# Performance work log

Hardware: AMD Instinct MI355X
Metric: run time of the kernel (lower is better)

The kernel has to match this reference:

```python
import jax, jax.numpy as jnp
import numpy as np

V = 16000      # vocab_size
D = 256        # embedding_dim
H = 512        # hidden_size (bi-LSTM concat)
HD = H // 2    # per-direction hidden
LAB = 32       # labelset_size (30 tags + START/STOP)
T = 512        # seq length
B = 128        # batch
START = 30
STOP = 31
NEG = -10000.0


def setup_inputs() -> dict:
    key = jax.random.key(0)
    ks = jax.random.split(key, 16)
    sc = 0.05
    emb = jax.random.normal(ks[0], (V, D), jnp.float32) * 0.1
    W_ih_f = jax.random.normal(ks[1], (4 * HD, D), jnp.float32) * sc
    W_hh_f = jax.random.normal(ks[2], (4 * HD, HD), jnp.float32) * sc
    b_f = jax.random.normal(ks[3], (4 * HD,), jnp.float32) * sc  # b_ih + b_hh combined
    W_ih_b = jax.random.normal(ks[4], (4 * HD, D), jnp.float32) * sc
    W_hh_b = jax.random.normal(ks[5], (4 * HD, HD), jnp.float32) * sc
    b_b = jax.random.normal(ks[6], (4 * HD,), jnp.float32) * sc
    Wo = jax.random.normal(ks[7], (LAB, H), jnp.float32) * sc
    bo = jnp.zeros((LAB,), jnp.float32)
    transitions = jax.random.normal(ks[8], (LAB, LAB), jnp.float32)
    transitions = transitions.at[STOP, :].set(NEG).at[:, START].set(NEG)
    h0 = jax.random.normal(ks[9], (2, B, HD), jnp.float32)  # init_hidden() uses randn
    c0 = jax.random.normal(ks[10], (2, B, HD), jnp.float32)
    sentences = jax.random.randint(ks[11], (T, B), 0, V, dtype=jnp.int32)
    labels = jax.random.randint(ks[12], (T, B), 0, 30, dtype=jnp.int32)
    masks = jnp.ones((T, B), dtype=bool)
    return {"emb": emb, "W_ih_f": W_ih_f, "W_hh_f": W_hh_f, "b_f": b_f,
            "W_ih_b": W_ih_b, "W_hh_b": W_hh_b, "b_b": b_b,
            "Wo": Wo, "bo": bo, "transitions": transitions,
            "h0": h0, "c0": c0,
            "sentences": sentences, "labels": labels, "masks": masks}


def _lstm_dir(xproj, h0, c0, W_hh):
    # xproj: [T, B, 4*HD] precomputed input projection (+bias)
    def step(carry, xg):
        h, c = carry
        g = xg + h @ W_hh.T
        i, f, gg, o = jnp.split(g, 4, axis=-1)  # torch gate order i,f,g,o
        i = jax.nn.sigmoid(i); f = jax.nn.sigmoid(f)
        gg = jnp.tanh(gg); o = jax.nn.sigmoid(o)
        c = f * c + i * gg
        h = o * jnp.tanh(c)
        return (h, c), h
    _, hs = jax.lax.scan(step, (h0, c0), xproj)
    return hs  # [T, B, HD]


def reference(emb, W_ih_f, W_hh_f, b_f, W_ih_b, W_hh_b, b_b, Wo, bo,
              transitions, h0, c0, sentences, labels, masks):
    # ---- encoder (dropout omitted: eval-mode determinism) ----
    x = emb[sentences]                                   # [T, B, D]
    xf = jnp.einsum('tbd,gd->tbg', x, W_ih_f) + b_f
    hf = _lstm_dir(xf, h0[0], c0[0], W_hh_f)             # [T, B, HD]
    xb = jnp.einsum('tbd,gd->tbg', x, W_ih_b) + b_b
    hb = _lstm_dir(xb[::-1], h0[1], c0[1], W_hh_b)[::-1]
    out = jnp.concatenate([hf, hb], axis=-1)             # [T, B, H]
    feats = jnp.einsum('tbh,lh->tbl', out, Wo) + bo      # [T, B, LAB]

    # ---- CRF forward algorithm (log partition) ----
    dp0 = jnp.full((B, LAB), NEG, jnp.float32).at[:, START].set(0.0)
    def fstep(dp, inp):
        sc, m = inp  # sc: [B, LAB], m: [B]
        new = jax.scipy.special.logsumexp(
            dp[:, :, None] + transitions[None, :, :] + sc[:, None, :], axis=1)
        return jnp.where(m[:, None], new, dp), None
    dpZ, _ = jax.lax.scan(fstep, dp0, (feats, masks))
    Z = jax.scipy.special.logsumexp(dpZ, axis=1)         # [B]

    # ---- gold path score ----
    lab_ext = jnp.concatenate(
        [jnp.full((1, B), START, labels.dtype), labels], axis=0)  # [T+1, B]
    bidx = jnp.arange(B)
    def gstep(dp, inp):
        sc, m, lp, ln = inp
        tmp = dp + transitions[lp, ln] + sc[bidx, ln]
        return jnp.where(m, tmp, dp), None
    gold, _ = jax.lax.scan(gstep, jnp.zeros((B,), jnp.float32),
                           (feats, masks, lab_ext[:-1], lab_ext[1:]))

    return (Z - gold).sum() / B
```

## Files before the change

### kernel.cpp

```cpp
#include <hip/hip_runtime.h>
#include <stdint.h>

typedef __attribute__((ext_vector_type(8))) short short8;
typedef __attribute__((ext_vector_type(4))) float floatx4;
typedef __attribute__((ext_vector_type(8))) int intx8;
typedef __attribute__((ext_vector_type(2))) int intx2;
typedef unsigned int u32;
typedef unsigned short u16;
typedef unsigned long long u64;

#define NROW 65536
#define RING 32

#define OFF_TAGS  64
#define OFF_READY 256
#define OFF_WIH   8192
#define OFF_WHH8  1056768
#define OFF_WO    2105344
#define OFF_RING  2138112
#define OFF_OUT   19177472
#define OFF_FE    86286336
#define WS_NEED   94674944

__device__ __forceinline__ u16 f2bf(float f){
  union { float f; u32 u; } v; v.f = f;
  u32 u = v.u;
  return (u16)((u + 0x7FFFu + ((u >> 16) & 1u)) >> 16);
}
__device__ __forceinline__ float bf2f(u16 h){
  union { u32 u; float f; } v; v.u = ((u32)h) << 16; return v.f;
}
__device__ __forceinline__ u32 pack2(float a, float b){
  return (u32)f2bf(a) | ((u32)f2bf(b) << 16);
}
__device__ __forceinline__ u32 pk_fp8x4(float a, float b, float c, float d){
  u32 lo = __builtin_amdgcn_cvt_pk_fp8_f32(a, b, 0, false);
  return (u32)__builtin_amdgcn_cvt_pk_fp8_f32(c, d, lo, true);
}
__device__ __forceinline__ float sigm(float x){
  return __builtin_amdgcn_rcpf(1.f + __expf(-x));
}
__device__ __forceinline__ float tanh_(float x){
  return 1.f - 2.f * __builtin_amdgcn_rcpf(1.f + __expf(2.f * x));
}
__device__ __forceinline__ floatx4 MF(short8 a, short8 b, floatx4 c){
  return __builtin_amdgcn_mfma_f32_16x16x32_bf16(a, b, c, 0, 0, 0);
}
__device__ __forceinline__ floatx4 MFS(intx8 a, intx8 b, floatx4 c){
  return __builtin_amdgcn_mfma_scale_f32_16x16x128_f8f6f4(
      a, b, c, 0, 0, 0, 0x7F7F7F7F, 0, 0x7F7F7F7F);
}
template<int CTRL>
__device__ __forceinline__ u32 dppq(u32 x){
  return (u32)__builtin_amdgcn_update_dpp(0, (int)x, CTRL, 0xF, 0xF, false);
}
__device__ __forceinline__ void ldsload16(const void* g, void* l){
  __builtin_amdgcn_global_load_lds(
      (const __attribute__((address_space(1))) u32*)g,
      (__attribute__((address_space(3))) u32*)l, 16, 0, 17);
}

__global__ void kdiag(float* out, float v){
  if (threadIdx.x == 0 && blockIdx.x == 0) out[0] = v;
}

__global__ void k0(const float* wf, const float* wb, const float* hf, const float* hb,
                   const float* wo, u16* wih, u16* wob, unsigned char* whh8){
  int e = blockIdx.x * 256 + threadIdx.x;
  if (e < 524288){ wih[e] = f2bf(e < 262144 ? wf[e] : wb[e - 262144]); return; }
  if (e < 540672){ wob[e - 524288] = f2bf(wo[e - 524288]); return; }
  if (e < 1064960){
    int t = e - 540672;
    float w = (t < 262144) ? hf[t] : hb[t - 262144];
    whh8[t] = (unsigned char)(__builtin_amdgcn_cvt_pk_fp8_f32(w, w, 0, false) & 0xFF);
  }
}

__global__ void __launch_bounds__(1024) __attribute__((amdgpu_waves_per_eu(4, 4)))
klstm(const float* emb, const int* sent, const u16* wih,
      const float* bf_, const float* bb_,
      const unsigned char* whh8, const float* h0, const float* c0,
      char* ring, u16* outb, u32* ct, u32* ready){
  __shared__ __align__(16) char SH[98304];
  const int tid = threadIdx.x, w = tid >> 6, l = tid & 63, q = l >> 4, l15 = l & 15;
  const int bid = blockIdx.x;

  if (bid >= 32){
    const int p = bid - 32, dir = p & 1;
    const float* bias = dir ? bb_ : bf_;
    const int m = w & 7, ch = w >> 3;
    int pbud = 1 << 20;
    for (int u = p; u < 1024; u += 224){
      const int s = u >> 1;
      const int t = dir ? 511 - s : s;
      if (s >= 31){
        const int li = l, need = s - 30;
        bool done = false;
        while (!done && pbud > 0){
          int v = need;
          if (li < 16)
            v = (int)__hip_atomic_load(&ct[dir * 16 + li], __ATOMIC_RELAXED, __HIP_MEMORY_SCOPE_AGENT);
          done = (__ballot(v >= need) == ~0ull);
          if (!done){ __builtin_amdgcn_s_sleep(32); pbud--; }
        }
      }
      {
        int r = tid >> 3, g0 = tid & 7;
        const float* er = emb + (size_t)sent[t * 128 + r] * 256;
        #pragma unroll
        for (int j = 0; j < 4; j++){
          int g8 = g0 + j * 8;
          float4 a = *(const float4*)(er + g8 * 8);
          float4 b = *(const float4*)(er + g8 * 8 + 4);
          u32 gg[4] = { pack2(a.x, a.y), pack2(a.z, a.w), pack2(b.x, b.y), pack2(b.z, b.w) };
          *(uint4*)&SH[(g8 * 128 + r) * 16] = *(uint4*)gg;
        }
      }
      __syncthreads();
      short8 Afr[8];
      #pragma unroll
      for (int ks = 0; ks < 8; ks++)
        Afr[ks] = *(const short8*)&SH[((ks * 4 + q) * 128 + m * 16 + l15) * 16];
      char* slot = ring + (size_t)(dir * RING + (s & (RING - 1))) * 262144;
      const int bcw = m * 2 + (q >> 1);
      for (int nt = 0; nt < 16; nt++){
        __syncthreads();
        {
          int r = tid & 63, grp = tid >> 6;
          const u16* wsrc = wih + (size_t)(dir * 1024 + nt * 64 + r) * 256;
          #pragma unroll
          for (int i = 0; i < 2; i++){
            int kg = grp * 2 + i;
            uint4 v = *(const uint4*)(wsrc + kg * 8);
            *(uint4*)&SH[65536 + (kg * 64 + r) * 16] = v;
          }
        }
        __syncthreads();
        floatx4 acc[2];
        acc[0] = floatx4{0.f,0.f,0.f,0.f};
        acc[1] = floatx4{0.f,0.f,0.f,0.f};
        #pragma unroll
        for (int ks = 0; ks < 8; ks++){
          #pragma unroll
          for (int jt = 0; jt < 2; jt++){
            short8 b = *(const short8*)&SH[65536 + ((ks * 4 + q) * 64 + ch * 32 + jt * 16 + l15) * 16];
            acc[jt] = MF(Afr[ks], b, acc[jt]);
          }
        }
        #pragma unroll
        for (int jt = 0; jt < 2; jt++){
          int col = nt * 64 + ch * 32 + jt * 16 + l15;
          float bv = bias[col];
          u32 pr[2] = { pack2(acc[jt][0] + bv, acc[jt][1] + bv),
                        pack2(acc[jt][2] + bv, acc[jt][3] + bv) };
          *(uint2*)(slot + bcw * 16384 + col * 16 + (q & 1) * 8) = *(uint2*)pr;
        }
      }
      asm volatile("s_waitcnt vmcnt(0)" ::: "memory");
      __syncthreads();
      if (tid == 0){
        __builtin_amdgcn_fence(__ATOMIC_RELEASE, "agent");
        __hip_atomic_store(&ready[dir * 512 + s], 1u, __ATOMIC_RELAXED, __HIP_MEMORY_SCOPE_AGENT);
      }
    }
    return;
  }

  const int dir = bid >> 4, bc = bid & 15;
  const int nn = w >> 1, hw = w & 1;
  const int H0 = nn * 32 + hw * 16, hid = H0 + l15;
  const int b0loc = (q & 1) * 4 + (q >> 1) * 2;
  const int i4 = l15 & 3, j4 = l15 >> 2;
  int cbud = 1 << 22;
  const u32 s01 = i4==0?0x00000400u : i4==1?0x00000105u : i4==2?0x06020000u : 0x03070000u;
  const u32 s23 = i4==0?0x04000000u : i4==1?0x01050000u : i4==2?0x00000602u : 0x00000307u;
  const u32 sfn = (i4 < 2) ? 0x07060100u : 0x03020504u;

  intx8 Wf[4][2];
  #pragma unroll
  for (int g = 0; g < 4; g++){
    const unsigned char* wr = whh8 + (size_t)(dir * 1024 + g * 256 + hid) * 256;
    #pragma unroll
    for (int i = 0; i < 2; i++)
      Wf[g][i] = *(const intx8*)(wr + i * 128 + q * 32);
  }
  #pragma unroll
  for (int g = 0; g < 4; g++){
    #pragma unroll
    for (int i = 0; i < 2; i++)
      asm volatile("" : "+v"(Wf[g][i]));
  }
  float creg[2];
  #pragma unroll
  for (int e = 0; e < 2; e++)
    creg[e] = c0[((size_t)dir * 128 + bc * 8 + b0loc + e) * 256 + hid];
  {
    int a = tid * 4;
    int kg = a >> 7, rest = a & 127, b = rest >> 3, off4 = a & 4;
    u32 val0 = 0;
    if (b < 8){
      const float* hr = h0 + ((size_t)dir * 128 + bc * 8 + b) * 256 + kg * 8 + off4;
      val0 = pk_fp8x4(hr[0], hr[1], hr[2], hr[3]);
    }
    *(u32*)&SH[49152 + a] = val0;
    *(u32*)&SH[49152 + 4096 + a] = 0;
  }
  #pragma unroll
  for (int pp = 0; pp < 2; pp++){
    while (__hip_atomic_load(&ready[dir * 512 + pp], __ATOMIC_RELAXED, __HIP_MEMORY_SCOPE_AGENT) == 0u
           && --cbud > 0)
      __builtin_amdgcn_s_sleep(8);
    const char* rp = ring + (size_t)(dir * RING + pp) * 262144 + bc * 16384;
    ldsload16(rp + tid * 16, SH + pp * 16384 + tid * 16);
  }
  u32 rdyv = __hip_atomic_load(&ready[dir * 512 + 2], __ATOMIC_RELAXED, __HIP_MEMORY_SCOPE_AGENT);
  asm volatile("s_waitcnt vmcnt(0)" ::: "memory");
  __syncthreads();

  int xcur = 0, xn2 = 2;
  for (int s = 0; s < 512; s++){
    const int t = dir ? 511 - s : s;
    u32 rdyn = 1u;
    if (s + 3 < 512)
      rdyn = __hip_atomic_load(&ready[dir * 512 + s + 3], __ATOMIC_RELAXED, __HIP_MEMORY_SCOPE_AGENT);
    if (s + 2 < 512){
      if (rdyv == 0u){
        while (__hip_atomic_load(&ready[dir * 512 + s + 2], __ATOMIC_RELAXED, __HIP_MEMORY_SCOPE_AGENT) == 0u
               && --cbud > 0)
          __builtin_amdgcn_s_sleep(2);
      }
      const char* rp = ring + (size_t)(dir * RING + ((s + 2) & (RING - 1))) * 262144 + bc * 16384;
      ldsload16(rp + tid * 16, SH + xn2 * 16384 + tid * 16);
    }
    rdyv = rdyn;

    const char* xb0 = SH + xcur * 16384;
    u32 xg[4];
    #pragma unroll
    for (int g = 0; g < 4; g++)
      xg[g] = *(const u32*)(xb0 + ((g * 256 + hid) * 16 + b0loc * 2));

    const char* hb = SH + 49152 + (s & 1) * 4096;
    floatx4 acc[4];
    #pragma unroll
    for (int g = 0; g < 4; g++) acc[g] = floatx4{0.f,0.f,0.f,0.f};
    #pragma unroll
    for (int i = 0; i < 2; i++){
      union { long l[4]; intx8 v; } au;
      #pragma unroll
      for (int j = 0; j < 4; j++)
        au.l[j] = *(const long*)(hb + ((i * 16 + q * 4 + j) * 16 + l15) * 8);
      #pragma unroll
      for (int g = 0; g < 4; g++)
        acc[g] = MFS(au.v, Wf[g][i], acc[g]);
    }

    float v[4][2];
    #pragma unroll
    for (int g = 0; g < 4; g++)
      #pragma unroll
      for (int e = 0; e < 2; e++){
        union { float f; int i; } lo, hi;
        lo.f = acc[g][e]; hi.f = acc[g][2 + e];
        intx2 r = __builtin_amdgcn_permlane32_swap(lo.i, hi.i, false, false);
        union { int i; float f; } o; o.i = r[0];
        v[g][e] = o.f;
      }

    float hv[2];
    #pragma unroll
    for (int e = 0; e < 2; e++){
      float gi = v[0][e] + bf2f((u16)(xg[0] >> (16 * e)));
      float gf = v[1][e] + bf2f((u16)(xg[1] >> (16 * e)));
      float gg = v[2][e] + bf2f((u16)(xg[2] >> (16 * e)));
      float go = v[3][e] + bf2f((u16)(xg[3] >> (16 * e)));
      gi = sigm(gi); gf = sigm(gf); gg = tanh_(gg); go = sigm(go);
      float c = gf * creg[e] + gi * gg;
      creg[e] = c;
      hv[e] = go * tanh_(c);
      outb[((size_t)t * 128 + bc * 8 + b0loc + e) * 512 + dir * 256 + hid] = f2bf(hv[e]);
    }

    {
      u32 pk = (u32)__builtin_amdgcn_cvt_pk_fp8_f32(hv[0], hv[1], 0, false);
      intx2 rq = __builtin_amdgcn_permlane32_swap((int)pk, (int)pk, false, false);
      u32 quad = (u32)rq[0] | ((u32)rq[1] << 16);
      u32 r1 = dppq<0xB1>(quad);
      u32 r2 = dppq<0x4E>(quad);
      u32 r3 = dppq<0x1B>(quad);
      u32 p01 = __builtin_amdgcn_perm(r1, quad, s01);
      u32 p23 = __builtin_amdgcn_perm(r3, r2, s23);
      u32 outw = __builtin_amdgcn_perm(p23, p01, sfn);
      char* hn = SH + 49152 + ((s + 1) & 1) * 4096;
      if (q < 2){
        int bq = q * 4 + i4;
        int hidg = H0 + j4 * 4;
        *(u32*)&hn[(hidg >> 3) * 128 + bq * 8 + (hidg & 4)] = outw;
      }
    }
    if (tid == 0)
      __hip_atomic_store(&ct[dir * 16 + bc], (u32)(s + 1), __ATOMIC_RELAXED, __HIP_MEMORY_SCOPE_AGENT);

    if (s < 509){
      asm volatile("s_waitcnt vmcnt(4) lgkmcnt(0)" ::: "memory");
      __builtin_amdgcn_s_barrier();
    } else if (s < 511){
      asm volatile("s_waitcnt vmcnt(0)" ::: "memory");
      __syncthreads();
    }
    xcur = (xcur == 2) ? 0 : xcur + 1;
    xn2  = (xn2  == 2) ? 0 : xn2  + 1;
  }
}

__launch_bounds__(256, 2)
__global__ void k5(const u16* outb, const u16* wob, const float* bo, float* fe){
  const int tid = threadIdx.x, w = tid >> 6, l15 = tid & 15, q = (tid >> 4) & 3;
  const int rows0 = blockIdx.x * 64;
  short8 WoF[2][16];
  #pragma unroll
  for (int jt = 0; jt < 2; jt++)
    #pragma unroll
    for (int ks = 0; ks < 16; ks++)
      WoF[jt][ks] = *(const short8*)(wob + (size_t)(jt * 16 + l15) * 512 + ks * 32 + q * 8);
  floatx4 a5[2] = { floatx4{0.f,0.f,0.f,0.f}, floatx4{0.f,0.f,0.f,0.f} };
  const u16* ar = outb + (size_t)(rows0 + w * 16 + l15) * 512;
  #pragma unroll
  for (int ks = 0; ks < 16; ks++){
    short8 a = *(const short8*)(ar + ks * 32 + q * 8);
    a5[0] = MF(a, WoF[0][ks], a5[0]);
    a5[1] = MF(a, WoF[1][ks], a5[1]);
  }
  #pragma unroll
  for (int jt = 0; jt < 2; jt++){
    float bv = bo[jt * 16 + l15];
    #pragma unroll
    for (int rg = 0; rg < 4; rg++)
      fe[(size_t)(rows0 + w * 16 + q * 4 + rg) * 32 + jt * 16 + l15] = a5[jt][rg] + bv;
  }
}

__global__ void k6(const float* fe, const int* labels, const float* trans, float* accp){
  __shared__ float TrL[1024];
  __shared__ __align__(16) float dpL[4][32];
  const int tid = threadIdx.x, w = tid >> 6, l = tid & 63, j = l & 31, half = l >> 5;
  const int b = blockIdx.x * 4 + w;
  for (int i = tid; i < 1024; i += 256) TrL[i] = trans[i];
  __syncthreads();
  float Trl[16];
  #pragma unroll
  for (int ii = 0; ii < 16; ii++) Trl[ii] = TrL[(half * 16 + ii) * 32 + j];
  if (half == 0) dpL[w][j] = (j == 30) ? 0.f : -10000.f;

  float gold = 0.f; int lp = 30;
  float sc = fe[(size_t)b * 32 + j];
  int lab = labels[b];
  float ndF = 0.f;
  for (int t = 0; t < 512; t++){
    float scN = 0.f; int labN = 0;
    if (t < 511){
      scN = fe[((size_t)(t + 1) * 128 + b) * 32 + j];
      labN = labels[(t + 1) * 128 + b];
    }
    float dpv[16], tt[16];
    {
      const float4 a = *(const float4*)&dpL[w][half * 16 + 0];
      const float4 b4 = *(const float4*)&dpL[w][half * 16 + 4];
      const float4 c4 = *(const float4*)&dpL[w][half * 16 + 8];
      const float4 d4 = *(const float4*)&dpL[w][half * 16 + 12];
      dpv[0]=a.x; dpv[1]=a.y; dpv[2]=a.z; dpv[3]=a.w;
      dpv[4]=b4.x; dpv[5]=b4.y; dpv[6]=b4.z; dpv[7]=b4.w;
      dpv[8]=c4.x; dpv[9]=c4.y; dpv[10]=c4.z; dpv[11]=c4.w;
      dpv[12]=d4.x; dpv[13]=d4.y; dpv[14]=d4.z; dpv[15]=d4.w;
    }
    float m = -3.0e38f;
    #pragma unroll
    for (int ii = 0; ii < 16; ii++){ tt[ii] = dpv[ii] + Trl[ii]; m = fmaxf(m, tt[ii]); }
    float M = fmaxf(m, __shfl_xor(m, 32));
    float ssum = 0.f;
    #pragma unroll
    for (int ii = 0; ii < 16; ii++) ssum += __expf(tt[ii] - M);
    ssum += __shfl_xor(ssum, 32);
    float nd = sc + M + __logf(ssum);
    float scl = __shfl(sc, lab);
    gold += TrL[lp * 32 + lab] + scl;
    lp = lab;
    if (half == 0) dpL[w][j] = nd;
    ndF = nd;
    sc = scN; lab = labN;
  }
  float M2 = ndF, S2 = 1.f;
  #pragma unroll
  for (int off = 1; off < 64; off <<= 1){
    float Mo = __shfl_xor(M2, off), So = __shfl_xor(S2, off);
    float Mn = fmaxf(M2, Mo);
    S2 = S2 * __expf(M2 - Mn) + So * __expf(Mo - Mn);
    M2 = Mn;
  }
  float Z = M2 + __logf(S2 * 0.5f);
  if (l == 0) atomicAdd(accp, Z - gold);
}

__global__ void k7(const float* accp, float* out){
  if (threadIdx.x == 0 && blockIdx.x == 0) out[0] = accp[0] * (1.f / 128.f);
}

extern "C" void kernel_launch(void* const* d_in, const int* in_sizes, int n_in,
                              void* d_out, int out_size, void* d_ws, size_t ws_size,
                              hipStream_t stream){
  float* outp = (float*)d_out;
  if (ws_size < (size_t)WS_NEED){
    hipLaunchKernelGGL(kdiag, dim3(1), dim3(64), 0, stream, outp, (float)ws_size);
    return;
  }
  const float* emb  = (const float*)d_in[0];
  const float* Wihf = (const float*)d_in[1];
  const float* Whhf = (const float*)d_in[2];
  const float* bf_  = (const float*)d_in[3];
  const float* Wihb = (const float*)d_in[4];
  const float* Whhb = (const float*)d_in[5];
  const float* bb_  = (const float*)d_in[6];
  const float* Wo   = (const float*)d_in[7];
  const float* bo   = (const float*)d_in[8];
  const float* trans= (const float*)d_in[9];
  const float* h0   = (const float*)d_in[10];
  const float* c0   = (const float*)d_in[11];
  const int*   sent = (const int*)d_in[12];
  const int*   labels = (const int*)d_in[13];

  char* ws = (char*)d_ws;
  float* accp = (float*)ws;
  u32* ct    = (u32*)(ws + OFF_TAGS);
  u32* ready = (u32*)(ws + OFF_READY);
  u16* wih   = (u16*)(ws + OFF_WIH);
  unsigned char* whh8 = (unsigned char*)(ws + OFF_WHH8);
  u16* wob   = (u16*)(ws + OFF_WO);
  char* ring = ws + OFF_RING;
  u16* outb  = (u16*)(ws + OFF_OUT);
  float* fe  = (float*)(ws + OFF_FE);

  hipMemsetAsync(d_ws, 0, 8192, stream);
  hipLaunchKernelGGL(k0, dim3(4160), dim3(256), 0, stream,
                     Wihf, Wihb, Whhf, Whhb, Wo, wih, wob, whh8);
  hipLaunchKernelGGL(klstm, dim3(256), dim3(1024), 0, stream,
                     emb, sent, wih, bf_, bb_, whh8, h0, c0, ring, outb, ct, ready);
  hipLaunchKernelGGL(k5, dim3(1024), dim3(256), 0, stream, outb, wob, bo, fe);
  hipLaunchKernelGGL(k6, dim3(32), dim3(256), 0, stream, fe, labels, trans, accp);
  hipLaunchKernelGGL(k7, dim3(1), dim3(64), 0, stream, accp, outp);
}
```

Baseline: 1.370 ms.

## Load LSTM input projections directly into registers instead of staging through LDS

The producer now writes the precomputed input-gate projections in a per-lane layout (hidden unit × batch-pair, with the four gates contiguous), so each recurrent-step lane can fetch its four gate words straight from the global ring with system-scope atomic loads. The old path, which used a global-to-LDS async copy into three rotating LDS buffers followed by LDS reads, is removed, and the prefetch distance drops from two steps to one. The aim is to take the LDS staging and its read latency off the serial recurrence critical path. In exchange, each step issues more small global loads with less lookahead, and the vmcnt wait accounting has been changed to match.

Result: slower. 1.922 ms (+40.3%).

```diff
diff --git a/kernel.cpp b/kernel.cpp
--- a/kernel.cpp
+++ b/kernel.cpp
@@ -54,10 +54,8 @@
 __device__ __forceinline__ u32 dppq(u32 x){
   return (u32)__builtin_amdgcn_update_dpp(0, (int)x, CTRL, 0xF, 0xF, false);
 }
-__device__ __forceinline__ void ldsload16(const void* g, void* l){
-  __builtin_amdgcn_global_load_lds(
-      (const __attribute__((address_space(1))) u32*)g,
-      (__attribute__((address_space(3))) u32*)l, 16, 0, 17);
+__device__ __forceinline__ u32 ldsys(const u32* p){
+  return __hip_atomic_load(p, __ATOMIC_RELAXED, __HIP_MEMORY_SCOPE_SYSTEM);
 }
 
 __global__ void kdiag(float* out, float v){
@@ -151,9 +149,11 @@
         for (int jt = 0; jt < 2; jt++){
           int col = nt * 64 + ch * 32 + jt * 16 + l15;
           float bv = bias[col];
-          u32 pr[2] = { pack2(acc[jt][0] + bv, acc[jt][1] + bv),
-                        pack2(acc[jt][2] + bv, acc[jt][3] + bv) };
-          *(uint2*)(slot + bcw * 16384 + col * 16 + (q & 1) * 8) = *(uint2*)pr;
+          u32 lo = pack2(acc[jt][0] + bv, acc[jt][1] + bv);
+          u32 hi = pack2(acc[jt][2] + bv, acc[jt][3] + bv);
+          char* base = slot + bcw * 16384 + (size_t)(col & 255) * 64 + (col >> 8) * 4;
+          *(u32*)(base + ((q & 1) * 2 + 0) * 16) = lo;
+          *(u32*)(base + ((q & 1) * 2 + 1) * 16) = hi;
         }
       }
       asm volatile("s_waitcnt vmcnt(0)" ::: "memory");
@@ -170,6 +170,7 @@
   const int nn = w >> 1, hw = w & 1;
   const int H0 = nn * 32 + hw * 16, hid = H0 + l15;
   const int b0loc = (q & 1) * 4 + (q >> 1) * 2;
+  const int bpair = b0loc >> 1;
   const int i4 = l15 & 3, j4 = l15 >> 2;
   int cbud = 1 << 22;
   const u32 s01 = i4==0?0x00000400u : i4==1?0x00000105u : i4==2?0x06020000u : 0x03070000u;
@@ -205,40 +206,37 @@
     *(u32*)&SH[49152 + a] = val0;
     *(u32*)&SH[49152 + 4096 + a] = 0;
   }
-  #pragma unroll
-  for (int pp = 0; pp < 2; pp++){
-    while (__hip_atomic_load(&ready[dir * 512 + pp], __ATOMIC_RELAXED, __HIP_MEMORY_SCOPE_AGENT) == 0u
-           && --cbud > 0)
-      __builtin_amdgcn_s_sleep(8);
-    const char* rp = ring + (size_t)(dir * RING + pp) * 262144 + bc * 16384;
-    ldsload16(rp + tid * 16, SH + pp * 16384 + tid * 16);
-  }
-  u32 rdyv = __hip_atomic_load(&ready[dir * 512 + 2], __ATOMIC_RELAXED, __HIP_MEMORY_SCOPE_AGENT);
+  const size_t lane_off = (size_t)bc * 16384 + (size_t)hid * 64 + (size_t)bpair * 16;
+  while (__hip_atomic_load(&ready[dir * 512 + 0], __ATOMIC_RELAXED, __HIP_MEMORY_SCOPE_AGENT) == 0u
+         && --cbud > 0)
+    __builtin_amdgcn_s_sleep(8);
+  u32 xg[4];
+  {
+    const u32* xp = (const u32*)(ring + (size_t)(dir * RING + 0) * 262144 + lane_off);
+    #pragma unroll
+    for (int g = 0; g < 4; g++) xg[g] = ldsys(xp + g);
+  }
+  u32 rdyv = __hip_atomic_load(&ready[dir * 512 + 1], __ATOMIC_RELAXED, __HIP_MEMORY_SCOPE_AGENT);
   asm volatile("s_waitcnt vmcnt(0)" ::: "memory");
   __syncthreads();
 
-  int xcur = 0, xn2 = 2;
   for (int s = 0; s < 512; s++){
     const int t = dir ? 511 - s : s;
     u32 rdyn = 1u;
-    if (s + 3 < 512)
-      rdyn = __hip_atomic_load(&ready[dir * 512 + s + 3], __ATOMIC_RELAXED, __HIP_MEMORY_SCOPE_AGENT);
-    if (s + 2 < 512){
+    if (s + 2 < 512)
+      rdyn = __hip_atomic_load(&ready[dir * 512 + s + 2], __ATOMIC_RELAXED, __HIP_MEMORY_SCOPE_AGENT);
+    u32 xn[4] = {0u, 0u, 0u, 0u};
+    if (s + 1 < 512){
       if (rdyv == 0u){
-        while (__hip_atomic_load(&ready[dir * 512 + s + 2], __ATOMIC_RELAXED, __HIP_MEMORY_SCOPE_AGENT) == 0u
+        while (__hip_atomic_load(&ready[dir * 512 + s + 1], __ATOMIC_RELAXED, __HIP_MEMORY_SCOPE_AGENT) == 0u
                && --cbud > 0)
           __builtin_amdgcn_s_sleep(2);
       }
-      const char* rp = ring + (size_t)(dir * RING + ((s + 2) & (RING - 1))) * 262144 + bc * 16384;
-      ldsload16(rp + tid * 16, SH + xn2 * 16384 + tid * 16);
+      const u32* xp = (const u32*)(ring + (size_t)(dir * RING + ((s + 1) & (RING - 1))) * 262144 + lane_off);
+      #pragma unroll
+      for (int g = 0; g < 4; g++) xn[g] = ldsys(xp + g);
     }
     rdyv = rdyn;
-
-    const char* xb0 = SH + xcur * 16384;
-    u32 xg[4];
-    #pragma unroll
-    for (int g = 0; g < 4; g++)
-      xg[g] = *(const u32*)(xb0 + ((g * 256 + hid) * 16 + b0loc * 2));
 
     const char* hb = SH + 49152 + (s & 1) * 4096;
     floatx4 acc[4];
@@ -301,15 +299,15 @@
     if (tid == 0)
       __hip_atomic_store(&ct[dir * 16 + bc], (u32)(s + 1), __ATOMIC_RELAXED, __HIP_MEMORY_SCOPE_AGENT);
 
-    if (s < 509){
-      asm volatile("s_waitcnt vmcnt(4) lgkmcnt(0)" ::: "memory");
+    if (s < 510){
+      asm volatile("s_waitcnt vmcnt(2) lgkmcnt(0)" ::: "memory");
       __builtin_amdgcn_s_barrier();
     } else if (s < 511){
       asm volatile("s_waitcnt vmcnt(0)" ::: "memory");
       __syncthreads();
     }
-    xcur = (xcur == 2) ? 0 : xcur + 1;
-    xn2  = (xn2  == 2) ? 0 : xn2  + 1;
+    #pragma unroll
+    for (int g = 0; g < 4; g++) xg[g] = xn[g];
   }
 }
 
```

## Split LSTM recurrence across 64 blocks with 4 batch rows each

Applied to the files above, without the earlier changes.

The recurrent LSTM blocks are doubled from 32 to 64, so each block handles 4 batch rows per direction instead of 8. The ring layout for the input projection changes to per-4-row sub-slots of 8 KB, and each lane now computes one hidden/batch element. That removes the permlane32 swaps and the complex perm shuffle used to repack h. The projection producer blocks shrink from 224 to 192 and wait on 32 counters per direction. Each recurrent step now does less serial work per block, at the cost of fewer producer blocks, wasted MFMA lanes on padded rows, and more synchronisation counters.

Result: slower. 2.707 ms (+97.7%).

```diff
diff --git a/kernel.cpp b/kernel.cpp
--- a/kernel.cpp
+++ b/kernel.cpp
@@ -4,16 +4,14 @@
 typedef __attribute__((ext_vector_type(8))) short short8;
 typedef __attribute__((ext_vector_type(4))) float floatx4;
 typedef __attribute__((ext_vector_type(8))) int intx8;
-typedef __attribute__((ext_vector_type(2))) int intx2;
 typedef unsigned int u32;
 typedef unsigned short u16;
 typedef unsigned long long u64;
 
-#define NROW 65536
 #define RING 32
 
 #define OFF_TAGS  64
-#define OFF_READY 256
+#define OFF_READY 512
 #define OFF_WIH   8192
 #define OFF_WHH8  1056768
 #define OFF_WO    2105344
@@ -85,12 +83,12 @@
   const int tid = threadIdx.x, w = tid >> 6, l = tid & 63, q = l >> 4, l15 = l & 15;
   const int bid = blockIdx.x;
 
-  if (bid >= 32){
-    const int p = bid - 32, dir = p & 1;
+  if (bid >= 64){
+    const int p = bid - 64, dir = p & 1;
     const float* bias = dir ? bb_ : bf_;
     const int m = w & 7, ch = w >> 3;
     int pbud = 1 << 20;
-    for (int u = p; u < 1024; u += 224){
+    for (int u = p; u < 1024; u += 192){
       const int s = u >> 1;
       const int t = dir ? 511 - s : s;
       if (s >= 31){
@@ -98,8 +96,8 @@
         bool done = false;
         while (!done && pbud > 0){
           int v = need;
-          if (li < 16)
-            v = (int)__hip_atomic_load(&ct[dir * 16 + li], __ATOMIC_RELAXED, __HIP_MEMORY_SCOPE_AGENT);
+          if (li < 32)
+            v = (int)__hip_atomic_load(&ct[dir * 32 + li], __ATOMIC_RELAXED, __HIP_MEMORY_SCOPE_AGENT);
           done = (__ballot(v >= need) == ~0ull);
           if (!done){ __builtin_amdgcn_s_sleep(32); pbud--; }
         }
@@ -122,7 +120,7 @@
       for (int ks = 0; ks < 8; ks++)
         Afr[ks] = *(const short8*)&SH[((ks * 4 + q) * 128 + m * 16 + l15) * 16];
       char* slot = ring + (size_t)(dir * RING + (s & (RING - 1))) * 262144;
-      const int bcw = m * 2 + (q >> 1);
+      const int sub2 = (m * 2 + (q >> 1)) * 2 + (q & 1);
       for (int nt = 0; nt < 16; nt++){
         __syncthreads();
         {
@@ -153,7 +151,7 @@
           float bv = bias[col];
           u32 pr[2] = { pack2(acc[jt][0] + bv, acc[jt][1] + bv),
                         pack2(acc[jt][2] + bv, acc[jt][3] + bv) };
-          *(uint2*)(slot + bcw * 16384 + col * 16 + (q & 1) * 8) = *(uint2*)pr;
+          *(uint2*)(slot + (size_t)sub2 * 8192 + col * 8) = *(uint2*)pr;
         }
       }
       asm volatile("s_waitcnt vmcnt(0)" ::: "memory");
@@ -166,15 +164,11 @@
     return;
   }
 
-  const int dir = bid >> 4, bc = bid & 15;
+  const int dir = bid >> 5, sub = bid & 31, bc = sub >> 1, half = sub & 1;
   const int nn = w >> 1, hw = w & 1;
   const int H0 = nn * 32 + hw * 16, hid = H0 + l15;
-  const int b0loc = (q & 1) * 4 + (q >> 1) * 2;
   const int i4 = l15 & 3, j4 = l15 >> 2;
   int cbud = 1 << 22;
-  const u32 s01 = i4==0?0x00000400u : i4==1?0x00000105u : i4==2?0x06020000u : 0x03070000u;
-  const u32 s23 = i4==0?0x04000000u : i4==1?0x01050000u : i4==2?0x00000602u : 0x00000307u;
-  const u32 sfn = (i4 < 2) ? 0x07060100u : 0x03020504u;
 
   intx8 Wf[4][2];
   #pragma unroll
@@ -190,36 +184,40 @@
     for (int i = 0; i < 2; i++)
       asm volatile("" : "+v"(Wf[g][i]));
   }
-  float creg[2];
-  #pragma unroll
-  for (int e = 0; e < 2; e++)
-    creg[e] = c0[((size_t)dir * 128 + bc * 8 + b0loc + e) * 256 + hid];
+  float creg = c0[((size_t)dir * 128 + bc * 8 + half * 4 + q) * 256 + hid];
   {
     int a = tid * 4;
-    int kg = a >> 7, rest = a & 127, b = rest >> 3, off4 = a & 4;
+    int kg = a >> 7, rest = a & 127, slot = rest >> 3, off4 = a & 4;
     u32 val0 = 0;
-    if (b < 8){
-      const float* hr = h0 + ((size_t)dir * 128 + bc * 8 + b) * 256 + kg * 8 + off4;
+    if ((slot & 3) == 0){
+      int r = slot >> 2;
+      const float* hr = h0 + ((size_t)dir * 128 + bc * 8 + half * 4 + r) * 256 + kg * 8 + off4;
       val0 = pk_fp8x4(hr[0], hr[1], hr[2], hr[3]);
     }
-    *(u32*)&SH[49152 + a] = val0;
-    *(u32*)&SH[49152 + 4096 + a] = 0;
-  }
+    *(u32*)&SH[24576 + a] = val0;
+    *(u32*)&SH[24576 + 4096 + a] = 0;
+  }
+  const size_t sub_off = (size_t)sub * 8192;
   #pragma unroll
   for (int pp = 0; pp < 2; pp++){
     while (__hip_atomic_load(&ready[dir * 512 + pp], __ATOMIC_RELAXED, __HIP_MEMORY_SCOPE_AGENT) == 0u
            && --cbud > 0)
       __builtin_amdgcn_s_sleep(8);
-    const char* rp = ring + (size_t)(dir * RING + pp) * 262144 + bc * 16384;
-    ldsload16(rp + tid * 16, SH + pp * 16384 + tid * 16);
+    if (tid < 512){
+      const char* rp = ring + (size_t)(dir * RING + pp) * 262144 + sub_off;
+      ldsload16(rp + tid * 16, SH + pp * 8192 + tid * 16);
+    }
   }
   u32 rdyv = __hip_atomic_load(&ready[dir * 512 + 2], __ATOMIC_RELAXED, __HIP_MEMORY_SCOPE_AGENT);
   asm volatile("s_waitcnt vmcnt(0)" ::: "memory");
   __syncthreads();
 
+  u16* op = outb + (size_t)(dir ? 511 : 0) * 65536
+            + (size_t)(bc * 8 + half * 4 + q) * 512 + dir * 256 + hid;
+  const ptrdiff_t dstep = dir ? -65536 : 65536;
+
   int xcur = 0, xn2 = 2;
   for (int s = 0; s < 512; s++){
-    const int t = dir ? 511 - s : s;
     u32 rdyn = 1u;
     if (s + 3 < 512)
       rdyn = __hip_atomic_load(&ready[dir * 512 + s + 3], __ATOMIC_RELAXED, __HIP_MEMORY_SCOPE_AGENT);
@@ -229,18 +227,20 @@
                && --cbud > 0)
           __builtin_amdgcn_s_sleep(2);
       }
-      const char* rp = ring + (size_t)(dir * RING + ((s + 2) & (RING - 1))) * 262144 + bc * 16384;
-      ldsload16(rp + tid * 16, SH + xn2 * 16384 + tid * 16);
+      if (tid < 512){
+        const char* rp = ring + (size_t)(dir * RING + ((s + 2) & (RING - 1))) * 262144 + sub_off;
+        ldsload16(rp + tid * 16, SH + xn2 * 8192 + tid * 16);
+      }
     }
     rdyv = rdyn;
 
-    const char* xb0 = SH + xcur * 16384;
-    u32 xg[4];
-    #pragma unroll
-    for (int g = 0; g < 4; g++)
-      xg[g] = *(const u32*)(xb0 + ((g * 256 + hid) * 16 + b0loc * 2));
-
-    const char* hb = SH + 49152 + (s & 1) * 4096;
+    const char* xb = SH + xcur * 8192 + hid * 8 + q * 2;
+    u32 x0 = *(const u16*)(xb + 0);
+    u32 x1 = *(const u16*)(xb + 2048);
+    u32 x2 = *(const u16*)(xb + 4096);
+    u32 x3 = *(const u16*)(xb + 6144);
+
+    const char* hb = SH + 24576 + (s & 1) * 4096;
     floatx4 acc[4];
     #pragma unroll
     for (int g = 0; g < 4; g++) acc[g] = floatx4{0.f,0.f,0.f,0.f};
@@ -255,54 +255,35 @@
         acc[g] = MFS(au.v, Wf[g][i], acc[g]);
     }
 
-    float v[4][2];
-    #pragma unroll
-    for (int g = 0; g < 4; g++)
-      #pragma unroll
-      for (int e = 0; e < 2; e++){
-        union { float f; int i; } lo, hi;
-        lo.f = acc[g][e]; hi.f = acc[g][2 + e];
-        intx2 r = __builtin_amdgcn_permlane32_swap(lo.i, hi.i, false, false);
-        union { int i; float f; } o; o.i = r[0];
-        v[g][e] = o.f;
-      }
-
-    float hv[2];
-    #pragma unroll
-    for (int e = 0; e < 2; e++){
-      float gi = v[0][e] + bf2f((u16)(xg[0] >> (16 * e)));
-      float gf = v[1][e] + bf2f((u16)(xg[1] >> (16 * e)));
-      float gg = v[2][e] + bf2f((u16)(xg[2] >> (16 * e)));
-      float go = v[3][e] + bf2f((u16)(xg[3] >> (16 * e)));
-      gi = sigm(gi); gf = sigm(gf); gg = tanh_(gg); go = sigm(go);
-      float c = gf * creg[e] + gi * gg;
-      creg[e] = c;
-      hv[e] = go * tanh_(c);
-      outb[((size_t)t * 128 + bc * 8 + b0loc + e) * 512 + dir * 256 + hid] = f2bf(hv[e]);
-    }
+    float gi = acc[0][0] + bf2f((u16)x0);
+    float gf = acc[1][0] + bf2f((u16)x1);
+    float gg = acc[2][0] + bf2f((u16)x2);
+    float go = acc[3][0] + bf2f((u16)x3);
+    gi = sigm(gi); gf = sigm(gf); gg = tanh_(gg); go = sigm(go);
+    float c = gf * creg + gi * gg;
+    creg = c;
+    float hv = go * tanh_(c);
+    *op = f2bf(hv);
+    op += dstep;
 
     {
-      u32 pk = (u32)__builtin_amdgcn_cvt_pk_fp8_f32(hv[0], hv[1], 0, false);
-      intx2 rq = __builtin_amdgcn_permlane32_swap((int)pk, (int)pk, false, false);
-      u32 quad = (u32)rq[0] | ((u32)rq[1] << 16);
-      u32 r1 = dppq<0xB1>(quad);
-      u32 r2 = dppq<0x4E>(quad);
-      u32 r3 = dppq<0x1B>(quad);
-      u32 p01 = __builtin_amdgcn_perm(r1, quad, s01);
-      u32 p23 = __builtin_amdgcn_perm(r3, r2, s23);
-      u32 outw = __builtin_amdgcn_perm(p23, p01, sfn);
-      char* hn = SH + 49152 + ((s + 1) & 1) * 4096;
-      if (q < 2){
-        int bq = q * 4 + i4;
-        int hidg = H0 + j4 * 4;
-        *(u32*)&hn[(hidg >> 3) * 128 + bq * 8 + (hidg & 4)] = outw;
+      union { float f; u32 u; } hu; hu.f = hv;
+      u32 n1 = dppq<0xB1>(hu.u);
+      union { u32 u; float f; } n1f; n1f.u = n1;
+      u32 pk = (u32)__builtin_amdgcn_cvt_pk_fp8_f32(hv, n1f.f, 0, false);
+      u32 n2 = dppq<0x4E>(pk);
+      u32 outw = (pk & 0xFFFFu) | (n2 << 16);
+      char* hn = SH + 24576 + ((s + 1) & 1) * 4096;
+      if (i4 == 0){
+        int hid4 = H0 + j4 * 4;
+        *(u32*)&hn[(hid4 >> 3) * 128 + q * 32 + (hid4 & 4)] = outw;
       }
     }
     if (tid == 0)
-      __hip_atomic_store(&ct[dir * 16 + bc], (u32)(s + 1), __ATOMIC_RELAXED, __HIP_MEMORY_SCOPE_AGENT);
-
-    if (s < 509){
-      asm volatile("s_waitcnt vmcnt(4) lgkmcnt(0)" ::: "memory");
+      __hip_atomic_store(&ct[dir * 32 + sub], (u32)(s + 1), __ATOMIC_RELAXED, __HIP_MEMORY_SCOPE_AGENT);
+
+    if (s < 510){
+      asm volatile("s_waitcnt vmcnt(3) lgkmcnt(0)" ::: "memory");
       __builtin_amdgcn_s_barrier();
     } else if (s < 511){
       asm volatile("s_waitcnt vmcnt(0)" ::: "memory");
```
